# Kernel tuning notes

Hardware: AMD Instinct MI355X
Metric: run time of the kernel (lower is better)

## Reference

```python
import jax, jax.numpy as jnp
import numpy as np

B, N, D = 2, 50000, 16
E = N * D  # total flattened neighbor entries


def setup_inputs() -> dict:
    key = jax.random.key(0)
    k1, k2, k3, k4 = jax.random.split(key, 4)
    xyz1 = jax.random.normal(k1, (B, N, 3), dtype=jnp.float32)
    # deformed coordinates = rest + small displacement (realistic ARAP setting)
    xyz2 = xyz1 + 0.1 * jax.random.normal(k2, (B, N, 3), dtype=jnp.float32)
    neighborList = jax.random.randint(k3, (E,), 0, N, dtype=jnp.int32)
    numNeighbors = jnp.full((N,), D, dtype=jnp.int32)
    accnumNeighbors = jnp.concatenate(
        [jnp.zeros((1,), jnp.int32), jnp.cumsum(numNeighbors)[:-1].astype(jnp.int32)])
    weightMatrix = jax.random.uniform(k4, (E,), dtype=jnp.float32)
    eye9 = jnp.eye(3, dtype=jnp.float32).reshape(9)
    rotations = jnp.broadcast_to(eye9, (B, N, 9))
    return {
        "xyz1": xyz1, "xyz2": xyz2, "neighborList": neighborList,
        "numNeighbors": numNeighbors, "accnumNeighbors": accnumNeighbors,
        "weightMatrix": weightMatrix, "rotations": rotations, "arapWeight": 1,
    }


def _arap_rotations(xyz1, xyz2, neighborList, numNeighbors, weightMatrix):
    b, n, _ = xyz1.shape
    e = neighborList.shape[0]
    # CSR segment ids: vertex id owning each flattened neighbor entry
    seg = jnp.repeat(jnp.arange(n, dtype=jnp.int32), numNeighbors, total_repeat_length=e)
    d1 = xyz1[:, seg] - xyz1[:, neighborList]   # [B,E,3] rest-pose edge vectors
    d2 = xyz2[:, seg] - xyz2[:, neighborList]   # [B,E,3] deformed edge vectors
    # weighted covariance contributions S_e = w_e * d1 d2^T : [B,E,3,3]
    outer = weightMatrix[None, :, None, None] * d1[..., :, None] * d2[..., None, :]
    # per-vertex covariance S_i = sum_{j in N(i)} S_e : [B,N,3,3]
    S = jax.vmap(lambda o: jax.ops.segment_sum(o, seg, num_segments=n))(outer)
    # Procrustes fit: R = V U^T with reflection fix
    U, s, Vt = jnp.linalg.svd(S)
    V = jnp.swapaxes(Vt, -1, -2)
    Ut = jnp.swapaxes(U, -1, -2)
    R = V @ Ut
    det = jnp.linalg.det(R)                      # [B,N]
    V = V.at[..., :, 2].multiply(jnp.where(det < 0, -1.0, 1.0)[..., None])
    R = V @ Ut
    return R.reshape(b, n, 9)


def reference(xyz1, xyz2, neighborList, numNeighbors, accnumNeighbors,
              weightMatrix, rotations, arapWeight):
    # accnumNeighbors (prefix offsets), rotations (initial guess) and arapWeight
    # are consumed by the CUDA kernel for addressing / loss weighting but do not
    # change the fitted rotations; the math is the ARAP local step below.
    return _arap_rotations(xyz1, xyz2, neighborList, numNeighbors, weightMatrix)
```

## Files before the change

kernel.cpp:

```cpp
#include <hip/hip_runtime.h>
#include <hip/hip_bf16.h>


__global__ __launch_bounds__(256)
void prepack_kernel(const float* __restrict__ xyz1,
                    const float* __restrict__ xyz2,
                    float4* __restrict__ pk,
                    int total)
{
    int t = blockIdx.x * blockDim.x + threadIdx.x;
    if (t >= total) return;
    float4 a, c;
    a.x = xyz1[t * 3 + 0]; a.y = xyz1[t * 3 + 1]; a.z = xyz1[t * 3 + 2]; a.w = 0.f;
    c.x = xyz2[t * 3 + 0]; c.y = xyz2[t * 3 + 1]; c.z = xyz2[t * 3 + 2]; c.w = 0.f;
    pk[2 * (size_t)t + 0] = a;
    pk[2 * (size_t)t + 1] = c;
}

__global__ __launch_bounds__(256)
void arap_rot_kernel(const float4* __restrict__ pk,
                     const int*   __restrict__ nbr,
                     const int*   __restrict__ num,
                     const int*   __restrict__ acc,
                     const float* __restrict__ wgt,
                     float*       __restrict__ out,
                     int B, int N)
{
    int t = blockIdx.x * blockDim.x + threadIdx.x;
    int total = B * N;
    if (t >= total) return;
    int b = t / N;
    int i = t - b * N;

    const float4* base = pk + 2 * (size_t)b * N;

    float4 P1 = base[2 * i + 0];
    float4 P2 = base[2 * i + 1];
    float p1x = P1.x, p1y = P1.y, p1z = P1.z;
    float p2x = P2.x, p2y = P2.y, p2z = P2.z;

    float Sxx = 0.f, Sxy = 0.f, Sxz = 0.f;
    float Syx = 0.f, Syy = 0.f, Syz = 0.f;
    float Szx = 0.f, Szy = 0.f, Szz = 0.f;

    int a0  = acc[i];
    int cnt = num[i];

    if (cnt == 16 && (a0 & 3) == 0) {
        const int4*   nb4 = (const int4*)(nbr + a0);
        const float4* w4  = (const float4*)(wgt + a0);
#pragma unroll
        for (int c = 0; c < 4; ++c) {
            int4   jj = nb4[c];
            float4 ww = w4[c];
            int js[4] = {jj.x, jj.y, jj.z, jj.w};
            float ws[4] = {ww.x, ww.y, ww.z, ww.w};
#pragma unroll
            for (int u = 0; u < 4; ++u) {
                int j = js[u];
                float4 A = base[2 * j + 0];
                float4 C = base[2 * j + 1];
                float we = ws[u];
                float d1x = p1x - A.x, d1y = p1y - A.y, d1z = p1z - A.z;
                float d2x = p2x - C.x, d2y = p2y - C.y, d2z = p2z - C.z;
                float w1x = we * d1x, w1y = we * d1y, w1z = we * d1z;
                Sxx += w1x * d2x;  Sxy += w1x * d2y;  Sxz += w1x * d2z;
                Syx += w1y * d2x;  Syy += w1y * d2y;  Syz += w1y * d2z;
                Szx += w1z * d2x;  Szy += w1z * d2y;  Szz += w1z * d2z;
            }
        }
    } else {
        for (int k = 0; k < cnt; ++k) {
            int   e  = a0 + k;
            int   j  = nbr[e];
            float we = wgt[e];
            float4 A = base[2 * j + 0];
            float4 C = base[2 * j + 1];
            float d1x = p1x - A.x, d1y = p1y - A.y, d1z = p1z - A.z;
            float d2x = p2x - C.x, d2y = p2y - C.y, d2z = p2z - C.z;
            float w1x = we * d1x, w1y = we * d1y, w1z = we * d1z;
            Sxx += w1x * d2x;  Sxy += w1x * d2y;  Sxz += w1x * d2z;
            Syx += w1y * d2x;  Syy += w1y * d2y;  Syz += w1y * d2z;
            Szx += w1z * d2x;  Szy += w1z * d2y;  Szz += w1z * d2z;
        }
    }

    float n00 =  Sxx + Syy + Szz;
    float n01 =  Syz - Szy;
    float n02 =  Szx - Sxz;
    float n03 =  Sxy - Syx;
    float n11 =  Sxx - Syy - Szz;
    float n12 =  Sxy + Syx;
    float n13 =  Szx + Sxz;
    float n22 = -Sxx + Syy - Szz;
    float n23 =  Syz + Szy;
    float n33 = -Sxx - Syy + Szz;

    float fro2 = Sxx*Sxx + Sxy*Sxy + Sxz*Sxz
               + Syx*Syx + Syy*Syy + Syz*Syz
               + Szx*Szx + Szy*Szy + Szz*Szz;
    float s = 2.0f * sqrtf(fro2) + 1e-30f;

    float m00 = n00 + s, m01 = n01, m02 = n02, m03 = n03;
    float m11 = n11 + s, m12 = n12, m13 = n13;
    float m22 = n22 + s, m23 = n23;
    float m33 = n33 + s;

    {
        float inv = 1.0f / (m00 + m11 + m22 + m33);
        m00 *= inv; m01 *= inv; m02 *= inv; m03 *= inv;
        m11 *= inv; m12 *= inv; m13 *= inv;
        m22 *= inv; m23 *= inv; m33 *= inv;
    }

#pragma unroll
    for (int it = 0; it < 16; ++it) {
        float p00 = m00*m00 + m01*m01 + m02*m02 + m03*m03;
        float p01 = m00*m01 + m01*m11 + m02*m12 + m03*m13;
        float p02 = m00*m02 + m01*m12 + m02*m22 + m03*m23;
        float p03 = m00*m03 + m01*m13 + m02*m23 + m03*m33;
        float p11 = m01*m01 + m11*m11 + m12*m12 + m13*m13;
        float p12 = m01*m02 + m11*m12 + m12*m22 + m13*m23;
        float p13 = m01*m03 + m11*m13 + m12*m23 + m13*m33;
        float p22 = m02*m02 + m12*m12 + m22*m22 + m23*m23;
        float p23 = m02*m03 + m12*m13 + m22*m23 + m23*m33;
        float p33 = m03*m03 + m13*m13 + m23*m23 + m33*m33;
        float inv = 1.0f / (p00 + p11 + p22 + p33);
        m00 = p00 * inv; m01 = p01 * inv; m02 = p02 * inv; m03 = p03 * inv;
        m11 = p11 * inv; m12 = p12 * inv; m13 = p13 * inv;
        m22 = p22 * inv; m23 = p23 * inv;
        m33 = p33 * inv;
    }

    float qw = m00, qx = m01, qy = m02, qz = m03, best = m00;
    {
        bool g = m11 > best;
        qw = g ? m01 : qw; qx = g ? m11 : qx; qy = g ? m12 : qy; qz = g ? m13 : qz;
        best = g ? m11 : best;
        g = m22 > best;
        qw = g ? m02 : qw; qx = g ? m12 : qx; qy = g ? m22 : qy; qz = g ? m23 : qz;
        best = g ? m22 : best;
        g = m33 > best;
        qw = g ? m03 : qw; qx = g ? m13 : qx; qy = g ? m23 : qy; qz = g ? m33 : qz;
    }
    {
        float inv = rsqrtf(qw*qw + qx*qx + qy*qy + qz*qz);
        qw *= inv; qx *= inv; qy *= inv; qz *= inv;
    }

    float xx = qx*qx, yy = qy*qy, zz = qz*qz;
    float xy = qx*qy, xz = qx*qz, yz = qy*qz;
    float wx = qw*qx, wy = qw*qy, wz = qw*qz;

    float* o = out + (size_t)t * 9;
    o[0] = 1.f - 2.f*(yy + zz);
    o[1] = 2.f*(xy - wz);
    o[2] = 2.f*(xz + wy);
    o[3] = 2.f*(xy + wz);
    o[4] = 1.f - 2.f*(xx + zz);
    o[5] = 2.f*(yz - wx);
    o[6] = 2.f*(xz - wy);
    o[7] = 2.f*(yz + wx);
    o[8] = 1.f - 2.f*(xx + yy);
}

extern "C" void kernel_launch(void* const* d_in, const int* in_sizes, int n_in,
                              void* d_out, int out_size, void* d_ws, size_t ws_size,
                              hipStream_t stream) {
    const float* xyz1 = (const float*)d_in[0];
    const float* xyz2 = (const float*)d_in[1];
    const int*   nbr  = (const int*)  d_in[2];
    const int*   num  = (const int*)  d_in[3];
    const int*   acc  = (const int*)  d_in[4];
    const float* wgt  = (const float*)d_in[5];
    float* out = (float*)d_out;

    int N = in_sizes[3];
    int B = in_sizes[0] / (N * 3);
    int total = B * N;

    float4* pk = (float4*)d_ws;

    int block = 256;
    int grid = (total + block - 1) / block;
    prepack_kernel<<<grid, block, 0, stream>>>(xyz1, xyz2, pk, total);
    arap_rot_kernel<<<grid, block, 0, stream>>>(pk, nbr, num, acc, wgt,
                                                out, B, N);
}
```

Before: 94.70 us.

## Split covariance gather across 16 lanes per vertex and separate eigen-solve kernel

Replaces the one-thread-per-vertex fused kernel with a gather kernel that assigns 16 lanes per vertex, one lane per neighbor, and reduces the 3x3 covariance with xor shuffles. The result is written in a structure-of-arrays layout to workspace. A separate solve kernel then reads it and runs the quaternion power iteration. The aim is more memory-level parallelism and coalesced neighbor and weight loads during the random gather. The cost is an extra kernel launch, a round trip of the covariance through global memory, and 16x more threads doing redundant center-point loads.

New measurement: 100.6 us. +6.2%, slower.

```diff
diff --git a/kernel.cpp b/kernel.cpp
--- a/kernel.cpp
+++ b/kernel.cpp
@@ -18,72 +18,73 @@
 }
 
 __global__ __launch_bounds__(256)
-void arap_rot_kernel(const float4* __restrict__ pk,
-                     const int*   __restrict__ nbr,
-                     const int*   __restrict__ num,
-                     const int*   __restrict__ acc,
-                     const float* __restrict__ wgt,
-                     float*       __restrict__ out,
-                     int B, int N)
+void gather_kernel(const float4* __restrict__ pk,
+                   const int*   __restrict__ nbr,
+                   const int*   __restrict__ num,
+                   const int*   __restrict__ acc,
+                   const float* __restrict__ wgt,
+                   float*       __restrict__ Sout,
+                   int B, int N)
 {
-    int t = blockIdx.x * blockDim.x + threadIdx.x;
+    int tid = blockIdx.x * blockDim.x + threadIdx.x;
+    int v = tid >> 4;
+    int k = tid & 15;
     int total = B * N;
-    if (t >= total) return;
-    int b = t / N;
-    int i = t - b * N;
+    if (v >= total) return;
+    int b = v / N;
+    int i = v - b * N;
 
     const float4* base = pk + 2 * (size_t)b * N;
-
     float4 P1 = base[2 * i + 0];
     float4 P2 = base[2 * i + 1];
-    float p1x = P1.x, p1y = P1.y, p1z = P1.z;
-    float p2x = P2.x, p2y = P2.y, p2z = P2.z;
+
+    int a0  = acc[i];
+    int cnt = num[i];
 
     float Sxx = 0.f, Sxy = 0.f, Sxz = 0.f;
     float Syx = 0.f, Syy = 0.f, Syz = 0.f;
     float Szx = 0.f, Szy = 0.f, Szz = 0.f;
 
-    int a0  = acc[i];
-    int cnt = num[i];
+    for (int kk = k; kk < cnt; kk += 16) {
+        int   e  = a0 + kk;
+        int   j  = nbr[e];
+        float we = wgt[e];
+        float4 A = base[2 * j + 0];
+        float4 C = base[2 * j + 1];
+        float d1x = P1.x - A.x, d1y = P1.y - A.y, d1z = P1.z - A.z;
+        float d2x = P2.x - C.x, d2y = P2.y - C.y, d2z = P2.z - C.z;
+        float w1x = we * d1x, w1y = we * d1y, w1z = we * d1z;
+        Sxx += w1x * d2x;  Sxy += w1x * d2y;  Sxz += w1x * d2z;
+        Syx += w1y * d2x;  Syy += w1y * d2y;  Syz += w1y * d2z;
+        Szx += w1z * d2x;  Szy += w1z * d2y;  Szz += w1z * d2z;
+    }
 
-    if (cnt == 16 && (a0 & 3) == 0) {
-        const int4*   nb4 = (const int4*)(nbr + a0);
-        const float4* w4  = (const float4*)(wgt + a0);
 #pragma unroll
-        for (int c = 0; c < 4; ++c) {
-            int4   jj = nb4[c];
-            float4 ww = w4[c];
-            int js[4] = {jj.x, jj.y, jj.z, jj.w};
-            float ws[4] = {ww.x, ww.y, ww.z, ww.w};
-#pragma unroll
-            for (int u = 0; u < 4; ++u) {
-                int j = js[u];
-                float4 A = base[2 * j + 0];
-                float4 C = base[2 * j + 1];
-                float we = ws[u];
-                float d1x = p1x - A.x, d1y = p1y - A.y, d1z = p1z - A.z;
-                float d2x = p2x - C.x, d2y = p2y - C.y, d2z = p2z - C.z;
-                float w1x = we * d1x, w1y = we * d1y, w1z = we * d1z;
-                Sxx += w1x * d2x;  Sxy += w1x * d2y;  Sxz += w1x * d2z;
-                Syx += w1y * d2x;  Syy += w1y * d2y;  Syz += w1y * d2z;
-                Szx += w1z * d2x;  Szy += w1z * d2y;  Szz += w1z * d2z;
-            }
-        }
-    } else {
-        for (int k = 0; k < cnt; ++k) {
-            int   e  = a0 + k;
-            int   j  = nbr[e];
-            float we = wgt[e];
-            float4 A = base[2 * j + 0];
-            float4 C = base[2 * j + 1];
-            float d1x = p1x - A.x, d1y = p1y - A.y, d1z = p1z - A.z;
-            float d2x = p2x - C.x, d2y = p2y - C.y, d2z = p2z - C.z;
-            float w1x = we * d1x, w1y = we * d1y, w1z = we * d1z;
-            Sxx += w1x * d2x;  Sxy += w1x * d2y;  Sxz += w1x * d2z;
-            Syx += w1y * d2x;  Syy += w1y * d2y;  Syz += w1y * d2z;
-            Szx += w1z * d2x;  Szy += w1z * d2y;  Szz += w1z * d2z;
-        }
+    for (int m = 8; m >= 1; m >>= 1) {
+        Sxx += __shfl_xor(Sxx, m);  Sxy += __shfl_xor(Sxy, m);  Sxz += __shfl_xor(Sxz, m);
+        Syx += __shfl_xor(Syx, m);  Syy += __shfl_xor(Syy, m);  Syz += __shfl_xor(Syz, m);
+        Szx += __shfl_xor(Szx, m);  Szy += __shfl_xor(Szy, m);  Szz += __shfl_xor(Szz, m);
     }
+
+    if (k == 0) {
+        size_t st = (size_t)total;
+        Sout[0 * st + v] = Sxx;  Sout[1 * st + v] = Sxy;  Sout[2 * st + v] = Sxz;
+        Sout[3 * st + v] = Syx;  Sout[4 * st + v] = Syy;  Sout[5 * st + v] = Syz;
+        Sout[6 * st + v] = Szx;  Sout[7 * st + v] = Szy;  Sout[8 * st + v] = Szz;
+    }
+}
+
+__global__ __launch_bounds__(256)
+void solve_kernel(const float* __restrict__ Sin,
+                  float*       __restrict__ out,
+                  int total)
+{
+    int t = blockIdx.x * blockDim.x + threadIdx.x;
+    if (t >= total) return;
+    size_t st = (size_t)total;
+    float Sxx = Sin[0 * st + t], Sxy = Sin[1 * st + t], Sxz = Sin[2 * st + t];
+    float Syx = Sin[3 * st + t], Syy = Sin[4 * st + t], Syz = Sin[5 * st + t];
+    float Szx = Sin[6 * st + t], Szy = Sin[7 * st + t], Szz = Sin[8 * st + t];
 
     float n00 =  Sxx + Syy + Szz;
     float n01 =  Syz - Szy;
@@ -180,10 +181,14 @@
     int total = B * N;
 
     float4* pk = (float4*)d_ws;
+    float*  Sb = (float*)((char*)d_ws + (size_t)total * 32);
 
     int block = 256;
-    int grid = (total + block - 1) / block;
-    prepack_kernel<<<grid, block, 0, stream>>>(xyz1, xyz2, pk, total);
-    arap_rot_kernel<<<grid, block, 0, stream>>>(pk, nbr, num, acc, wgt,
-                                                out, B, N);
+    prepack_kernel<<<(total + block - 1) / block, block, 0, stream>>>(
+        xyz1, xyz2, pk, total);
+    int gthreads = total * 16;
+    gather_kernel<<<(gthreads + block - 1) / block, block, 0, stream>>>(
+        pk, nbr, num, acc, wgt, Sb, B, N);
+    solve_kernel<<<(total + block - 1) / block, block, 0, stream>>>(
+        Sb, out, total);
 }
```
